# Performance work log

Hardware: AMD Instinct MI355X
Metric: run time of the kernel (lower is better)

Reference implementation:

```python
import jax, jax.numpy as jnp
import numpy as np

B = 262144
XD = 100
HID = 128
OUT = 1


def _dense_params(key, fan_in, fan_out):
    kw, _ = jax.random.split(key)
    limit = np.sqrt(6.0 / (fan_in + fan_out)).astype(np.float32)  # glorot uniform, Keras default
    w = jax.random.uniform(kw, (fan_in, fan_out), jnp.float32, -limit, limit)
    b = jnp.zeros((fan_out,), jnp.float32)
    return w, b


def setup_inputs() -> dict:
    key = jax.random.key(0)
    ks = jax.random.split(key, 13)
    x = jax.random.normal(ks[0], (B, XD), jnp.float32)
    t = jax.random.uniform(ks[1], (B, 1), jnp.float32)
    xt_dim = XD + 1
    Sw_w, Sw_b = _dense_params(ks[2], xt_dim, HID)
    Uz_w, Uz_b = _dense_params(ks[3], xt_dim, HID)
    Wsz_w, Wsz_b = _dense_params(ks[4], HID, HID)
    Ug_w, Ug_b = _dense_params(ks[5], xt_dim, HID)
    Wsg_w, Wsg_b = _dense_params(ks[6], HID, HID)
    Ur_w, Ur_b = _dense_params(ks[7], xt_dim, HID)
    Wsr_w, Wsr_b = _dense_params(ks[8], HID, HID)
    Uh_w, Uh_b = _dense_params(ks[9], xt_dim, HID)
    Wsh_w, Wsh_b = _dense_params(ks[10], HID, HID)
    Wf_w, Wf_b = _dense_params(ks[11], HID, OUT)
    return {
        "x": x, "t": t,
        "Sw_w": Sw_w, "Sw_b": Sw_b,
        "Uz_w": Uz_w, "Uz_b": Uz_b, "Wsz_w": Wsz_w, "Wsz_b": Wsz_b,
        "Ug_w": Ug_w, "Ug_b": Ug_b, "Wsg_w": Wsg_w, "Wsg_b": Wsg_b,
        "Ur_w": Ur_w, "Ur_b": Ur_b, "Wsr_w": Wsr_w, "Wsr_b": Wsr_b,
        "Uh_w": Uh_w, "Uh_b": Uh_b, "Wsh_w": Wsh_w, "Wsh_b": Wsh_b,
        "Wf_w": Wf_w, "Wf_b": Wf_b,
        "n_layers": 4,
    }


def reference(x, t, Sw_w, Sw_b, Uz_w, Uz_b, Wsz_w, Wsz_b, Ug_w, Ug_b,
              Wsg_w, Wsg_b, Ur_w, Ur_b, Wsr_w, Wsr_b, Uh_w, Uh_b,
              Wsh_w, Wsh_b, Wf_w, Wf_b, n_layers):
    xt = jnp.concatenate([x, t], axis=1)  # [B, XD+1]
    # Hoist xt projections out of the loop: xt is constant across depth steps.
    uz = xt @ Uz_w + Uz_b
    ug = xt @ Ug_w + Ug_b
    ur = xt @ Ur_w + Ur_b
    uh = xt @ Uh_w + Uh_b
    out = jnp.tanh(xt @ Sw_w + Sw_b)  # S1, [B, HID]
    for _ in range(1, int(n_layers)):
        S = out
        Z = jnp.tanh(uz + S @ Wsz_w + Wsz_b)
        G = jnp.tanh(ug + S @ Wsg_w + Wsg_b)
        R = jnp.tanh(ur + S @ Wsr_w + Wsr_b)
        H = uh + (S * R) @ Wsh_w + Wsh_b  # note: no tanh on H, as in source
        out = (1.0 - G) * H + Z * S
    return out @ Wf_w + Wf_b  # [B, OUT]
```

## Files before the change

### kernel.cpp

```cpp
#include <hip/hip_runtime.h>


typedef __attribute__((ext_vector_type(8))) short bf16x8;
typedef __attribute__((ext_vector_type(4))) float f32x4;
typedef __attribute__((ext_vector_type(4))) unsigned int u32x4;
typedef __attribute__((ext_vector_type(2))) unsigned int u32x2;

#define HID 128
#define XD 100
#define BROWS 32
#define NMAT 9
#define MATS 16384

__device__ __forceinline__ unsigned short f2bf(float f) {
    unsigned u = __float_as_uint(f);
    return (unsigned short)((u + 0x7FFFu + ((u >> 16) & 1u)) >> 16);
}
__device__ __forceinline__ unsigned pack2(float lo, float hi) {
    unsigned ul = __float_as_uint(lo), uh = __float_as_uint(hi);
    unsigned bl = (ul + 0x7FFFu + ((ul >> 16) & 1u)) >> 16;
    unsigned bh = (uh + 0x7FFFu + ((uh >> 16) & 1u)) & 0xFFFF0000u;
    return bl | bh;
}
__device__ __forceinline__ float bf_lo(unsigned p) { return __uint_as_float(p << 16); }
__device__ __forceinline__ float bf_hi(unsigned p) { return __uint_as_float(p & 0xFFFF0000u); }

__device__ __forceinline__ float fast_tanh(float x) {
    float e = __expf(2.0f * x);
    return 1.0f - 2.0f * __builtin_amdgcn_rcpf(e + 1.0f);
}
__device__ __forceinline__ float one_m_tanh(float x) {
    float e = __expf(2.0f * x);
    return 2.0f * __builtin_amdgcn_rcpf(e + 1.0f);
}

__global__ void prep_kernel(const float* __restrict__ Sw, const float* __restrict__ Uz,
                            const float* __restrict__ Ug, const float* __restrict__ Ur,
                            const float* __restrict__ Uh, const float* __restrict__ Wsz,
                            const float* __restrict__ Wsg, const float* __restrict__ Wsr,
                            const float* __restrict__ Wsh, unsigned short* __restrict__ out) {
    int g = blockIdx.x * blockDim.x + threadIdx.x;
    if (g >= NMAT * 4096) return;
    int m = g >> 12, r = g & 4095;
    int k = r >> 5, n4 = (r & 31) * 4;
    const float* src; int kmax;
    switch (m) {
        case 0: src = Sw;  kmax = 101; break;
        case 1: src = Uz;  kmax = 101; break;
        case 2: src = Ug;  kmax = 101; break;
        case 3: src = Ur;  kmax = 101; break;
        case 4: src = Uh;  kmax = 101; break;
        case 5: src = Wsz; kmax = 128; break;
        case 6: src = Wsg; kmax = 128; break;
        case 7: src = Wsr; kmax = 128; break;
        default: src = Wsh; kmax = 128; break;
    }
    f32x4 v = (f32x4){0.f, 0.f, 0.f, 0.f};
    if (k < kmax) v = *(const f32x4*)(src + k * HID + n4);
    int ks = k >> 5, b = k & 7, lq = ((k >> 3) & 3) << 4;
    int nt = n4 >> 4;
    size_t mb = (size_t)m * MATS;
    #pragma unroll
    for (int i = 0; i < 4; ++i) {
        int lane = lq | ((n4 + i) & 15);
        out[mb + (size_t)((ks * 8 + nt) * 64 + lane) * 8 + b] = f2bf(v[i]);
    }
}

__device__ __forceinline__ void gemm32(const unsigned short* __restrict__ A,
                                       const bf16x8 (&B)[4], int lane,
                                       f32x4 (&acc)[2]) {
    #pragma unroll
    for (int ks = 0; ks < 4; ++ks) {
        #pragma unroll
        for (int mt = 0; mt < 2; ++mt) {
            bf16x8 a = *(const bf16x8*)(A + mt * 2048 + ks * 512 + lane * 8);
            acc[mt] = __builtin_amdgcn_mfma_f32_16x16x32_bf16(a, B[ks], acc[mt], 0, 0, 0);
        }
    }
}

__device__ __forceinline__ void loadB(const unsigned short* __restrict__ wbuf, int mat,
                                      int nt, int lane, bf16x8 (&B)[4]) {
    #pragma unroll
    for (int ks = 0; ks < 4; ++ks)
        B[ks] = *(const bf16x8*)(wbuf + (size_t)mat * MATS +
                                 ((size_t)((ks * 8 + nt) * 64 + lane)) * 8);
}

__global__ __launch_bounds__(512, 4)
void dgm_main(const float* __restrict__ x, const float* __restrict__ tptr,
              const unsigned short* __restrict__ wbuf,
              const float* __restrict__ Sw_b, const float* __restrict__ Uz_b,
              const float* __restrict__ Ug_b, const float* __restrict__ Ur_b,
              const float* __restrict__ Uh_b,
              const float* __restrict__ Wsz_b, const float* __restrict__ Wsg_b,
              const float* __restrict__ Wsr_b, const float* __restrict__ Wsh_b,
              const float* __restrict__ Wf_w, const float* __restrict__ Wf_b,
              const int* __restrict__ nlayers, float* __restrict__ y) {
    __shared__ unsigned short lds[32768];
    unsigned short* xtb = lds;
    unsigned short* sb  = lds + 4096;

    const int tid = threadIdx.x;
    const int wv = tid >> 6, lane = tid & 63;
    const int quad = lane >> 4, l15 = lane & 15;
    const int blk = blockIdx.x;
    const int lcount = nlayers[0] - 1;
    const int nt = wv;

    const int col = nt * 16 + l15;
    const int sc = (col >> 5) * 512 + ((col >> 3) & 3) * 128 + (col & 7) + quad * 32;

    {
        int mt = tid >> 8;
        ((unsigned*)xtb)[mt * 1024 + 768 + (tid & 255)] = 0u;
    }
    __syncthreads();

    {
        const float* xsrc = x + (size_t)blk * BROWS * XD;
        for (int i = tid; i < BROWS * (XD / 4); i += 512) {
            int row = i / 25, c4 = i % 25, k0 = c4 * 4;
            f32x4 v = *(const f32x4*)(xsrc + row * XD + k0);
            int idx = (row >> 4) * 2048 + (k0 >> 5) * 512 + ((k0 >> 3) & 3) * 128 +
                      (row & 15) * 8 + (k0 & 7);
            *(u32x2*)(xtb + idx) = (u32x2){pack2(v[0], v[1]), pack2(v[2], v[3])};
        }
        if (tid < BROWS) {
            int idx = (tid >> 4) * 2048 + 3 * 512 + (tid & 15) * 8 + 4;
            xtb[idx] = f2bf(tptr[(size_t)blk * BROWS + tid]);
        }
    }
    __syncthreads();

    f32x4 acc[2];
    f32x4 sreg4[2];
    unsigned u2[4][2][2];
    bf16x8 Bcur[4], Bnxt[4];

    loadB(wbuf, 0, nt, lane, Bcur);
    {
        float bv = Sw_b[col];
        loadB(wbuf, 1, nt, lane, Bnxt);
        acc[0] = (f32x4){bv, bv, bv, bv};
        acc[1] = acc[0];
        gemm32(xtb, Bcur, lane, acc);
        #pragma unroll
        for (int mt = 0; mt < 2; ++mt) {
            f32x4 s;
            s[0] = fast_tanh(acc[mt][0]);
            s[1] = fast_tanh(acc[mt][1]);
            s[2] = fast_tanh(acc[mt][2]);
            s[3] = fast_tanh(acc[mt][3]);
            sreg4[mt] = s;
            unsigned p01 = pack2(s[0], s[1]), p23 = pack2(s[2], s[3]);
            int base = mt * 2048 + sc;
            sb[base + 0]  = (unsigned short)p01;
            sb[base + 8]  = (unsigned short)(p01 >> 16);
            sb[base + 16] = (unsigned short)p23;
            sb[base + 24] = (unsigned short)(p23 >> 16);
        }
    }
    {
        const float* ubias[4] = {Uz_b, Ug_b, Ur_b, Uh_b};
        #pragma unroll
        for (int mi = 0; mi < 4; ++mi) {
            #pragma unroll
            for (int ks = 0; ks < 4; ++ks)
                Bcur[ks] = Bnxt[ks];
            if (mi < 3) loadB(wbuf, mi + 2, nt, lane, Bnxt);
            float bv = ubias[mi][col];
            acc[0] = (f32x4){bv, bv, bv, bv};
            acc[1] = acc[0];
            gemm32(xtb, Bcur, lane, acc);
            u2[mi][0][0] = pack2(acc[0][0], acc[0][1]);
            u2[mi][0][1] = pack2(acc[0][2], acc[0][3]);
            u2[mi][1][0] = pack2(acc[1][0], acc[1][1]);
            u2[mi][1][1] = pack2(acc[1][2], acc[1][3]);
        }
    }
    __syncthreads();

    bf16x8 Wz[4], Wg[4], Wr[4], Wh[4];
    loadB(wbuf, 5, nt, lane, Wz);
    loadB(wbuf, 6, nt, lane, Wg);
    loadB(wbuf, 7, nt, lane, Wr);
    loadB(wbuf, 8, nt, lane, Wh);

    f32x4 tp4[2];
    f32x4 gp4[2];

    for (int l = 0; l < lcount; ++l) {
        #pragma unroll
        for (int mt = 0; mt < 2; ++mt)
            acc[mt] = (f32x4){bf_lo(u2[2][mt][0]), bf_hi(u2[2][mt][0]),
                              bf_lo(u2[2][mt][1]), bf_hi(u2[2][mt][1])};
        gemm32(sb, Wr, lane, acc);
        #pragma unroll
        for (int mt = 0; mt < 2; ++mt) {
            float q0 = sreg4[mt][0] * fast_tanh(acc[mt][0]);
            float q1 = sreg4[mt][1] * fast_tanh(acc[mt][1]);
            float q2 = sreg4[mt][2] * fast_tanh(acc[mt][2]);
            float q3 = sreg4[mt][3] * fast_tanh(acc[mt][3]);
            unsigned q01 = pack2(q0, q1), q23 = pack2(q2, q3);
            int base = mt * 2048 + sc;
            xtb[base + 0]  = (unsigned short)q01;
            xtb[base + 8]  = (unsigned short)(q01 >> 16);
            xtb[base + 16] = (unsigned short)q23;
            xtb[base + 24] = (unsigned short)(q23 >> 16);
        }
        __syncthreads();

        #pragma unroll
        for (int mt = 0; mt < 2; ++mt)
            acc[mt] = (f32x4){bf_lo(u2[0][mt][0]), bf_hi(u2[0][mt][0]),
                              bf_lo(u2[0][mt][1]), bf_hi(u2[0][mt][1])};
        gemm32(sb, Wz, lane, acc);
        #pragma unroll
        for (int mt = 0; mt < 2; ++mt) {
            tp4[mt][0] = fast_tanh(acc[mt][0]) * sreg4[mt][0];
            tp4[mt][1] = fast_tanh(acc[mt][1]) * sreg4[mt][1];
            tp4[mt][2] = fast_tanh(acc[mt][2]) * sreg4[mt][2];
            tp4[mt][3] = fast_tanh(acc[mt][3]) * sreg4[mt][3];
        }

        #pragma unroll
        for (int mt = 0; mt < 2; ++mt)
            acc[mt] = (f32x4){bf_lo(u2[1][mt][0]), bf_hi(u2[1][mt][0]),
                              bf_lo(u2[1][mt][1]), bf_hi(u2[1][mt][1])};
        gemm32(sb, Wg, lane, acc);
        #pragma unroll
        for (int mt = 0; mt < 2; ++mt) {
            gp4[mt][0] = one_m_tanh(acc[mt][0]);
            gp4[mt][1] = one_m_tanh(acc[mt][1]);
            gp4[mt][2] = one_m_tanh(acc[mt][2]);
            gp4[mt][3] = one_m_tanh(acc[mt][3]);
        }

        #pragma unroll
        for (int mt = 0; mt < 2; ++mt)
            acc[mt] = (f32x4){bf_lo(u2[3][mt][0]), bf_hi(u2[3][mt][0]),
                              bf_lo(u2[3][mt][1]), bf_hi(u2[3][mt][1])};
        gemm32(xtb, Wh, lane, acc);
        __syncthreads();
        bool lastl = (l == lcount - 1);
        #pragma unroll
        for (int mt = 0; mt < 2; ++mt) {
            f32x4 o;
            o[0] = gp4[mt][0] * acc[mt][0] + tp4[mt][0];
            o[1] = gp4[mt][1] * acc[mt][1] + tp4[mt][1];
            o[2] = gp4[mt][2] * acc[mt][2] + tp4[mt][2];
            o[3] = gp4[mt][3] * acc[mt][3] + tp4[mt][3];
            sreg4[mt] = o;
            if (!lastl) {
                unsigned p01 = pack2(o[0], o[1]), p23 = pack2(o[2], o[3]);
                int base = mt * 2048 + sc;
                sb[base + 0]  = (unsigned short)p01;
                sb[base + 8]  = (unsigned short)(p01 >> 16);
                sb[base + 16] = (unsigned short)p23;
                sb[base + 24] = (unsigned short)(p23 >> 16);
            }
        }
        if (!lastl) __syncthreads();
    }

    float* yp = (float*)xtb;
    float wfv = Wf_w[col];
    #pragma unroll
    for (int mt = 0; mt < 2; ++mt)
        #pragma unroll
        for (int e = 0; e < 4; ++e) {
            float p = sreg4[mt][e] * wfv;
            p += __shfl_xor(p, 1);
            p += __shfl_xor(p, 2);
            p += __shfl_xor(p, 4);
            p += __shfl_xor(p, 8);
            if (l15 == 0) yp[(mt * 16 + quad * 4 + e) * 8 + wv] = p;
        }
    __syncthreads();
    if (tid < BROWS) {
        const float* r8 = yp + tid * 8;
        float r = ((r8[0] + r8[1]) + (r8[2] + r8[3])) +
                  ((r8[4] + r8[5]) + (r8[6] + r8[7])) + Wf_b[0];
        y[(size_t)blk * BROWS + tid] = r;
    }
}

extern "C" void kernel_launch(void* const* d_in, const int* in_sizes, int n_in,
                              void* d_out, int out_size, void* d_ws, size_t ws_size,
                              hipStream_t stream) {
    const float* x     = (const float*)d_in[0];
    const float* t     = (const float*)d_in[1];
    const float* Sw_w  = (const float*)d_in[2];
    const float* Sw_b  = (const float*)d_in[3];
    const float* Uz_w  = (const float*)d_in[4];
    const float* Uz_b  = (const float*)d_in[5];
    const float* Wsz_w = (const float*)d_in[6];
    const float* Wsz_b = (const float*)d_in[7];
    const float* Ug_w  = (const float*)d_in[8];
    const float* Ug_b  = (const float*)d_in[9];
    const float* Wsg_w = (const float*)d_in[10];
    const float* Wsg_b = (const float*)d_in[11];
    const float* Ur_w  = (const float*)d_in[12];
    const float* Ur_b  = (const float*)d_in[13];
    const float* Wsr_w = (const float*)d_in[14];
    const float* Wsr_b = (const float*)d_in[15];
    const float* Uh_w  = (const float*)d_in[16];
    const float* Uh_b  = (const float*)d_in[17];
    const float* Wsh_w = (const float*)d_in[18];
    const float* Wsh_b = (const float*)d_in[19];
    const float* Wf_w  = (const float*)d_in[20];
    const float* Wf_b  = (const float*)d_in[21];
    const int*   nl    = (const int*)d_in[22];

    unsigned short* wbuf = (unsigned short*)d_ws;
    float* y = (float*)d_out;
    const int B = in_sizes[0] / XD;

    prep_kernel<<<dim3((NMAT * 4096 + 255) / 256), dim3(256), 0, stream>>>(
        Sw_w, Uz_w, Ug_w, Ur_w, Uh_w, Wsz_w, Wsg_w, Wsr_w, Wsh_w, wbuf);

    dgm_main<<<dim3(B / BROWS), dim3(512), 0, stream>>>(
        x, t, wbuf, Sw_b, Uz_b, Ug_b, Ur_b, Uh_b,
        Wsz_b, Wsg_b, Wsr_b, Wsh_b, Wf_w, Wf_b, nl, y);
}
```

Measured before the change: 378.3 us.

## Fold 2/ln2 into weights, merge Ws biases, and batch gate GEMMs per layer

Pre-scales the tanh-bound weights and biases by 2*log2(e) so each activation uses exp2 directly instead of exp with a multiply. The Ws* biases are folded into the hoisted U projections once instead of being dropped or re-added per layer. The R, Z and G recurrent GEMMs are interleaved in one pass that shares A-fragment loads, and the xt projections are done two at a time. Z/G intermediates are stored packed in bf16 to save registers, at some precision cost and with more live accumulators.

```diff
diff --git a/kernel.cpp b/kernel.cpp
--- a/kernel.cpp
+++ b/kernel.cpp
@@ -3,7 +3,6 @@
 
 typedef __attribute__((ext_vector_type(8))) short bf16x8;
 typedef __attribute__((ext_vector_type(4))) float f32x4;
-typedef __attribute__((ext_vector_type(4))) unsigned int u32x4;
 typedef __attribute__((ext_vector_type(2))) unsigned int u32x2;
 
 #define HID 128
@@ -11,6 +10,7 @@
 #define BROWS 32
 #define NMAT 9
 #define MATS 16384
+#define C2L 2.885390081777926815f
 
 __device__ __forceinline__ unsigned short f2bf(float f) {
     unsigned u = __float_as_uint(f);
@@ -25,12 +25,12 @@
 __device__ __forceinline__ float bf_lo(unsigned p) { return __uint_as_float(p << 16); }
 __device__ __forceinline__ float bf_hi(unsigned p) { return __uint_as_float(p & 0xFFFF0000u); }
 
-__device__ __forceinline__ float fast_tanh(float x) {
-    float e = __expf(2.0f * x);
+__device__ __forceinline__ float tanh_ps(float a) {
+    float e = __builtin_amdgcn_exp2f(a);
     return 1.0f - 2.0f * __builtin_amdgcn_rcpf(e + 1.0f);
 }
-__device__ __forceinline__ float one_m_tanh(float x) {
-    float e = __expf(2.0f * x);
+__device__ __forceinline__ float omt_ps(float a) {
+    float e = __builtin_amdgcn_exp2f(a);
     return 2.0f * __builtin_amdgcn_rcpf(e + 1.0f);
 }
 
@@ -55,6 +55,7 @@
         case 7: src = Wsr; kmax = 128; break;
         default: src = Wsh; kmax = 128; break;
     }
+    float sc = (m == 4 || m == 8) ? 1.0f : C2L;
     f32x4 v = (f32x4){0.f, 0.f, 0.f, 0.f};
     if (k < kmax) v = *(const f32x4*)(src + k * HID + n4);
     int ks = k >> 5, b = k & 7, lq = ((k >> 3) & 3) << 4;
@@ -63,7 +64,7 @@
     #pragma unroll
     for (int i = 0; i < 4; ++i) {
         int lane = lq | ((n4 + i) & 15);
-        out[mb + (size_t)((ks * 8 + nt) * 64 + lane) * 8 + b] = f2bf(v[i]);
+        out[mb + (size_t)((ks * 8 + nt) * 64 + lane) * 8 + b] = f2bf(v[i] * sc);
     }
 }
 
@@ -71,13 +72,38 @@
                                        const bf16x8 (&B)[4], int lane,
                                        f32x4 (&acc)[2]) {
     #pragma unroll
-    for (int ks = 0; ks < 4; ++ks) {
+    for (int ks = 0; ks < 4; ++ks)
         #pragma unroll
         for (int mt = 0; mt < 2; ++mt) {
             bf16x8 a = *(const bf16x8*)(A + mt * 2048 + ks * 512 + lane * 8);
             acc[mt] = __builtin_amdgcn_mfma_f32_16x16x32_bf16(a, B[ks], acc[mt], 0, 0, 0);
         }
-    }
+}
+__device__ __forceinline__ void gemm32x2(const unsigned short* __restrict__ A,
+                                         const bf16x8 (&B0)[4], const bf16x8 (&B1)[4],
+                                         int lane, f32x4 (&a0)[2], f32x4 (&a1)[2]) {
+    #pragma unroll
+    for (int ks = 0; ks < 4; ++ks)
+        #pragma unroll
+        for (int mt = 0; mt < 2; ++mt) {
+            bf16x8 a = *(const bf16x8*)(A + mt * 2048 + ks * 512 + lane * 8);
+            a0[mt] = __builtin_amdgcn_mfma_f32_16x16x32_bf16(a, B0[ks], a0[mt], 0, 0, 0);
+            a1[mt] = __builtin_amdgcn_mfma_f32_16x16x32_bf16(a, B1[ks], a1[mt], 0, 0, 0);
+        }
+}
+__device__ __forceinline__ void gemm32x3(const unsigned short* __restrict__ A,
+                                         const bf16x8 (&B0)[4], const bf16x8 (&B1)[4],
+                                         const bf16x8 (&B2)[4], int lane,
+                                         f32x4 (&a0)[2], f32x4 (&a1)[2], f32x4 (&a2)[2]) {
+    #pragma unroll
+    for (int ks = 0; ks < 4; ++ks)
+        #pragma unroll
+        for (int mt = 0; mt < 2; ++mt) {
+            bf16x8 a = *(const bf16x8*)(A + mt * 2048 + ks * 512 + lane * 8);
+            a0[mt] = __builtin_amdgcn_mfma_f32_16x16x32_bf16(a, B0[ks], a0[mt], 0, 0, 0);
+            a1[mt] = __builtin_amdgcn_mfma_f32_16x16x32_bf16(a, B1[ks], a1[mt], 0, 0, 0);
+            a2[mt] = __builtin_amdgcn_mfma_f32_16x16x32_bf16(a, B2[ks], a2[mt], 0, 0, 0);
+        }
 }
 
 __device__ __forceinline__ void loadB(const unsigned short* __restrict__ wbuf, int mat,
@@ -134,25 +160,23 @@
     }
     __syncthreads();
 
-    f32x4 acc[2];
     f32x4 sreg4[2];
     unsigned u2[4][2][2];
-    bf16x8 Bcur[4], Bnxt[4];
-
-    loadB(wbuf, 0, nt, lane, Bcur);
+
     {
-        float bv = Sw_b[col];
-        loadB(wbuf, 1, nt, lane, Bnxt);
-        acc[0] = (f32x4){bv, bv, bv, bv};
-        acc[1] = acc[0];
-        gemm32(xtb, Bcur, lane, acc);
+        bf16x8 Bq[4];
+        loadB(wbuf, 0, nt, lane, Bq);
+        float bv = Sw_b[col] * C2L;
+        f32x4 acc[2];
+        acc[0] = (f32x4){bv, bv, bv, bv}; acc[1] = acc[0];
+        gemm32(xtb, Bq, lane, acc);
         #pragma unroll
         for (int mt = 0; mt < 2; ++mt) {
             f32x4 s;
-            s[0] = fast_tanh(acc[mt][0]);
-            s[1] = fast_tanh(acc[mt][1]);
-            s[2] = fast_tanh(acc[mt][2]);
-            s[3] = fast_tanh(acc[mt][3]);
+            s[0] = tanh_ps(acc[mt][0]);
+            s[1] = tanh_ps(acc[mt][1]);
+            s[2] = tanh_ps(acc[mt][2]);
+            s[3] = tanh_ps(acc[mt][3]);
             sreg4[mt] = s;
             unsigned p01 = pack2(s[0], s[1]), p23 = pack2(s[2], s[3]);
             int base = mt * 2048 + sc;
@@ -163,21 +187,35 @@
         }
     }
     {
-        const float* ubias[4] = {Uz_b, Ug_b, Ur_b, Uh_b};
-        #pragma unroll
-        for (int mi = 0; mi < 4; ++mi) {
-            #pragma unroll
-            for (int ks = 0; ks < 4; ++ks)
-                Bcur[ks] = Bnxt[ks];
-            if (mi < 3) loadB(wbuf, mi + 2, nt, lane, Bnxt);
-            float bv = ubias[mi][col];
-            acc[0] = (f32x4){bv, bv, bv, bv};
-            acc[1] = acc[0];
-            gemm32(xtb, Bcur, lane, acc);
-            u2[mi][0][0] = pack2(acc[0][0], acc[0][1]);
-            u2[mi][0][1] = pack2(acc[0][2], acc[0][3]);
-            u2[mi][1][0] = pack2(acc[1][0], acc[1][1]);
-            u2[mi][1][1] = pack2(acc[1][2], acc[1][3]);
+        bf16x8 Ba[4], Bb[4];
+        f32x4 a0[2], a1[2];
+        loadB(wbuf, 1, nt, lane, Ba);
+        loadB(wbuf, 2, nt, lane, Bb);
+        float bz = (Uz_b[col] + Wsz_b[col]) * C2L;
+        float bg = (Ug_b[col] + Wsg_b[col]) * C2L;
+        a0[0] = (f32x4){bz, bz, bz, bz}; a0[1] = a0[0];
+        a1[0] = (f32x4){bg, bg, bg, bg}; a1[1] = a1[0];
+        gemm32x2(xtb, Ba, Bb, lane, a0, a1);
+        #pragma unroll
+        for (int mt = 0; mt < 2; ++mt) {
+            u2[0][mt][0] = pack2(a0[mt][0], a0[mt][1]);
+            u2[0][mt][1] = pack2(a0[mt][2], a0[mt][3]);
+            u2[1][mt][0] = pack2(a1[mt][0], a1[mt][1]);
+            u2[1][mt][1] = pack2(a1[mt][2], a1[mt][3]);
+        }
+        loadB(wbuf, 3, nt, lane, Ba);
+        loadB(wbuf, 4, nt, lane, Bb);
+        float br = (Ur_b[col] + Wsr_b[col]) * C2L;
+        float bh = Uh_b[col] + Wsh_b[col];
+        a0[0] = (f32x4){br, br, br, br}; a0[1] = a0[0];
+        a1[0] = (f32x4){bh, bh, bh, bh}; a1[1] = a1[0];
+        gemm32x2(xtb, Ba, Bb, lane, a0, a1);
+        #pragma unroll
+        for (int mt = 0; mt < 2; ++mt) {
+            u2[2][mt][0] = pack2(a0[mt][0], a0[mt][1]);
+            u2[2][mt][1] = pack2(a0[mt][2], a0[mt][3]);
+            u2[3][mt][0] = pack2(a1[mt][0], a1[mt][1]);
+            u2[3][mt][1] = pack2(a1[mt][2], a1[mt][3]);
         }
     }
     __syncthreads();
@@ -188,56 +226,43 @@
     loadB(wbuf, 7, nt, lane, Wr);
     loadB(wbuf, 8, nt, lane, Wh);
 
-    f32x4 tp4[2];
-    f32x4 gp4[2];
+    unsigned tp2[2][2];
+    unsigned gp2[2][2];
 
     for (int l = 0; l < lcount; ++l) {
-        #pragma unroll
-        for (int mt = 0; mt < 2; ++mt)
-            acc[mt] = (f32x4){bf_lo(u2[2][mt][0]), bf_hi(u2[2][mt][0]),
-                              bf_lo(u2[2][mt][1]), bf_hi(u2[2][mt][1])};
-        gemm32(sb, Wr, lane, acc);
-        #pragma unroll
-        for (int mt = 0; mt < 2; ++mt) {
-            float q0 = sreg4[mt][0] * fast_tanh(acc[mt][0]);
-            float q1 = sreg4[mt][1] * fast_tanh(acc[mt][1]);
-            float q2 = sreg4[mt][2] * fast_tanh(acc[mt][2]);
-            float q3 = sreg4[mt][3] * fast_tanh(acc[mt][3]);
+        f32x4 aR[2], aZ[2], aG[2];
+        #pragma unroll
+        for (int mt = 0; mt < 2; ++mt) {
+            aR[mt] = (f32x4){bf_lo(u2[2][mt][0]), bf_hi(u2[2][mt][0]),
+                             bf_lo(u2[2][mt][1]), bf_hi(u2[2][mt][1])};
+            aZ[mt] = (f32x4){bf_lo(u2[0][mt][0]), bf_hi(u2[0][mt][0]),
+                             bf_lo(u2[0][mt][1]), bf_hi(u2[0][mt][1])};
+            aG[mt] = (f32x4){bf_lo(u2[1][mt][0]), bf_hi(u2[1][mt][0]),
+                             bf_lo(u2[1][mt][1]), bf_hi(u2[1][mt][1])};
+        }
+        gemm32x3(sb, Wr, Wz, Wg, lane, aR, aZ, aG);
+        #pragma unroll
+        for (int mt = 0; mt < 2; ++mt) {
+            float q0 = sreg4[mt][0] * tanh_ps(aR[mt][0]);
+            float q1 = sreg4[mt][1] * tanh_ps(aR[mt][1]);
+            float q2 = sreg4[mt][2] * tanh_ps(aR[mt][2]);
+            float q3 = sreg4[mt][3] * tanh_ps(aR[mt][3]);
             unsigned q01 = pack2(q0, q1), q23 = pack2(q2, q3);
             int base = mt * 2048 + sc;
             xtb[base + 0]  = (unsigned short)q01;
             xtb[base + 8]  = (unsigned short)(q01 >> 16);
             xtb[base + 16] = (unsigned short)q23;
             xtb[base + 24] = (unsigned short)(q23 >> 16);
+            tp2[mt][0] = pack2(tanh_ps(aZ[mt][0]) * sreg4[mt][0],
+                               tanh_ps(aZ[mt][1]) * sreg4[mt][1]);
+            tp2[mt][1] = pack2(tanh_ps(aZ[mt][2]) * sreg4[mt][2],
+                               tanh_ps(aZ[mt][3]) * sreg4[mt][3]);
+            gp2[mt][0] = pack2(omt_ps(aG[mt][0]), omt_ps(aG[mt][1]));
+            gp2[mt][1] = pack2(omt_ps(aG[mt][2]), omt_ps(aG[mt][3]));
         }
         __syncthreads();
 
-        #pragma unroll
-        for (int mt = 0; mt < 2; ++mt)
-            acc[mt] = (f32x4){bf_lo(u2[0][mt][0]), bf_hi(u2[0][mt][0]),
-                              bf_lo(u2[0][mt][1]), bf_hi(u2[0][mt][1])};
-        gemm32(sb, Wz, lane, acc);
-        #pragma unroll
-        for (int mt = 0; mt < 2; ++mt) {
-            tp4[mt][0] = fast_tanh(acc[mt][0]) * sreg4[mt][0];
-            tp4[mt][1] = fast_tanh(acc[mt][1]) * sreg4[mt][1];
-            tp4[mt][2] = fast_tanh(acc[mt][2]) * sreg4[mt][2];
-            tp4[mt][3] = fast_tanh(acc[mt][3]) * sreg4[mt][3];
-        }
-
-        #pragma unroll
-        for (int mt = 0; mt < 2; ++mt)
-            acc[mt] = (f32x4){bf_lo(u2[1][mt][0]), bf_hi(u2[1][mt][0]),
-                              bf_lo(u2[1][mt][1]), bf_hi(u2[1][mt][1])};
-        gemm32(sb, Wg, lane, acc);
-        #pragma unroll
-        for (int mt = 0; mt < 2; ++mt) {
-            gp4[mt][0] = one_m_tanh(acc[mt][0]);
-            gp4[mt][1] = one_m_tanh(acc[mt][1]);
-            gp4[mt][2] = one_m_tanh(acc[mt][2]);
-            gp4[mt][3] = one_m_tanh(acc[mt][3]);
-        }
-
+        f32x4 acc[2];
         #pragma unroll
         for (int mt = 0; mt < 2; ++mt)
             acc[mt] = (f32x4){bf_lo(u2[3][mt][0]), bf_hi(u2[3][mt][0]),
@@ -248,10 +273,10 @@
         #pragma unroll
         for (int mt = 0; mt < 2; ++mt) {
             f32x4 o;
-            o[0] = gp4[mt][0] * acc[mt][0] + tp4[mt][0];
-            o[1] = gp4[mt][1] * acc[mt][1] + tp4[mt][1];
-            o[2] = gp4[mt][2] * acc[mt][2] + tp4[mt][2];
-            o[3] = gp4[mt][3] * acc[mt][3] + tp4[mt][3];
+            o[0] = bf_lo(gp2[mt][0]) * acc[mt][0] + bf_lo(tp2[mt][0]);
+            o[1] = bf_hi(gp2[mt][0]) * acc[mt][1] + bf_hi(tp2[mt][0]);
+            o[2] = bf_lo(gp2[mt][1]) * acc[mt][2] + bf_lo(tp2[mt][1]);
+            o[3] = bf_hi(gp2[mt][1]) * acc[mt][3] + bf_hi(tp2[mt][1]);
             sreg4[mt] = o;
             if (!lastl) {
                 unsigned p01 = pack2(o[0], o[1]), p23 = pack2(o[2], o[3]);
```

New measurement: 691.1 us. +82.7%, slower.
